# Kernel tuning notes

Hardware: AMD Instinct MI355X
Metric: run time of the kernel (lower is better)

The kernel has to match this reference:

```python
import jax, jax.numpy as jnp
import numpy as np

NEIGHBOUR = 3  # matches init_kwargs['neighbour']


def _conv2d(x, w, b=None, stride=1, pad=0):
    out = jax.lax.conv_general_dilated(
        x, w, (stride, stride), [(pad, pad), (pad, pad)],
        dimension_numbers=('NCHW', 'OIHW', 'NCHW'))
    if b is not None:
        out = out + b[None, :, None, None]
    return out


def _warp(x, offset, wg_w, wg_b, conv_w):
    """Deformable bilinear warp: offsets -> 4 corner gathers -> modulate -> regroup -> strided conv."""
    k = NEIGHBOUR
    N = k * k
    B, C, H, W = x.shape
    m = jax.nn.sigmoid(_conv2d(x, wg_w, wg_b, 1, 1))          # [B,N,H,W] modulation gate
    xp = jnp.pad(x, ((0, 0), (0, 0), (1, 1), (1, 1)))         # zero pad -> [B,C,H+2,W+2]
    Hp, Wp = H + 2, W + 2
    r = jnp.arange(-(k - 1) // 2, (k - 1) // 2 + 1, dtype=x.dtype)
    pnx, pny = jnp.meshgrid(r, r, indexing='ij')              # kernel-neighbour offsets p_n
    # absolute sampling positions in padded coords (p_0 starts at 1 due to padding)
    p0x = jnp.arange(1, H + 1, dtype=x.dtype)[None, :, None, None]
    p0y = jnp.arange(1, W + 1, dtype=x.dtype)[None, None, :, None]
    off = offset.transpose(0, 2, 3, 1)                        # [B,H,W,2N]; first N = x, last N = y
    px = p0x + pnx.ravel()[None, None, None, :] + off[..., :N]  # [B,H,W,N]
    py = p0y + pny.ravel()[None, None, None, :] + off[..., N:]
    fx = jnp.floor(jax.lax.stop_gradient(px))                 # p.detach().floor()
    fy = jnp.floor(jax.lax.stop_gradient(py))
    qx_lt = jnp.clip(fx, 0, Hp - 1)
    qy_lt = jnp.clip(fy, 0, Wp - 1)
    qx_rb = jnp.clip(fx + 1, 0, Hp - 1)
    qy_rb = jnp.clip(fy + 1, 0, Wp - 1)
    px = jnp.clip(px, 0, Hp - 1)
    py = jnp.clip(py, 0, Wp - 1)
    # bilinear weights (same algebra as the torch code)
    g_lt = (1 + (qx_lt - px)) * (1 + (qy_lt - py))
    g_rb = (1 - (qx_rb - px)) * (1 - (qy_rb - py))
    g_lb = (1 + (qx_lt - px)) * (1 - (qy_rb - py))
    g_rt = (1 - (qx_rb - px)) * (1 + (qy_lt - py))
    ix_lt = qx_lt.astype(jnp.int32); iy_lt = qy_lt.astype(jnp.int32)
    ix_rb = qx_rb.astype(jnp.int32); iy_rb = qy_rb.astype(jnp.int32)
    x_flat = xp.reshape(B, C, Hp * Wp)

    def gather(ix, iy):
        idx = (ix * Wp + iy).reshape(B, 1, H * W * N)
        return jnp.take_along_axis(x_flat, idx, axis=-1).reshape(B, C, H, W, N)

    xw = (g_lt[:, None] * gather(ix_lt, iy_lt)
          + g_rb[:, None] * gather(ix_rb, iy_rb)
          + g_lb[:, None] * gather(ix_lt, iy_rb)
          + g_rt[:, None] * gather(ix_rb, iy_lt))              # [B,C,H,W,N]
    xw = xw * m.transpose(0, 2, 3, 1)[:, None]                 # modulation, broadcast over C
    # regroup [B,C,H,W,k,k] -> [B,C,H*k,W*k] (matches _reshape_x_warped ordering)
    xw = xw.reshape(B, C, H, W, k, k).transpose(0, 1, 2, 4, 3, 5).reshape(B, C, H * k, W * k)
    return _conv2d(xw, conv_w, None, stride=k, pad=0)          # grouped-back strided conv


def setup_inputs() -> dict:
    B, C, MH, H, W = 4, 64, 18, 128, 128  # MH = 2*neighbour^2
    key = jax.random.key(0)
    ks = jax.random.split(key, 12)
    f32 = jnp.float32
    s = 0.05  # weight scale to keep gates unsaturated
    return {
        'x_t': jax.random.normal(ks[0], (B, C, H, W), f32),
        'pre_offset': jax.random.normal(ks[1], (B, MH, H, W), f32),
        'mean': jax.random.normal(ks[2], (B, MH, H, W), f32),
        'upd_w': s * jax.random.normal(ks[3], (MH, C + MH, 3, 3), f32),
        'upd_b': s * jax.random.normal(ks[4], (MH,), f32),
        'rst_w': s * jax.random.normal(ks[5], (MH, C + MH, 3, 3), f32),
        'rst_b': s * jax.random.normal(ks[6], (MH,), f32),
        'out_w': s * jax.random.normal(ks[7], (MH, C + MH, 3, 3), f32),
        'out_b': s * jax.random.normal(ks[8], (MH,), f32),
        'wg_w': s * jax.random.normal(ks[9], (9, C, 3, 3), f32),
        'wg_b': s * jax.random.normal(ks[10], (9,), f32),
        'warp_conv_w': s * jax.random.normal(ks[11], (C, C, 3, 3), f32),
    }


def reference(x_t, pre_offset, mean, upd_w, upd_b, rst_w, rst_b, out_w, out_b,
              wg_w, wg_b, warp_conv_w):
    stacked = jnp.concatenate([x_t, pre_offset], axis=1)
    update_gate = jax.nn.sigmoid(_conv2d(stacked, upd_w, upd_b, 1, 1))
    reset_gate = jax.nn.sigmoid(_conv2d(stacked, rst_w, rst_b, 1, 1))
    cand = jnp.tanh(_conv2d(jnp.concatenate([x_t, pre_offset * reset_gate], axis=1), out_w, out_b, 1, 1))
    offset = pre_offset * (1 - update_gate) + cand * update_gate
    mean_new = mean + 0.5 * (pre_offset - mean)
    offset = offset + mean_new
    x_out = _warp(x_t, offset, wg_w, wg_b, warp_conv_w)
    return (x_out, offset, mean_new)
```

## Files before the change

kernel.cpp:

```cpp
#include <hip/hip_runtime.h>
#include <hip/hip_bf16.h>
#include <math.h>

#define Bn  4
#define Cc  64
#define MHc 18
#define Hh  128
#define Wd  128
#define HW  (Hh*Wd)
#define Np  9
#define HP  130
#define WP  130
#define XPE (HP*WP*Cc)
#define PPE (HP*WP*32)
#define KX  576
#define KP  288
#define KT  (KX+KP)

typedef __attribute__((ext_vector_type(8))) short short8;
typedef __attribute__((ext_vector_type(4))) float float4v;

__device__ __forceinline__ float bf2f(__hip_bfloat16 x) { return __bfloat162float(x); }
__device__ __forceinline__ __hip_bfloat16 f2bf(float x) { return __float2bfloat16(x); }
__device__ __forceinline__ float sigm(float x) { return 1.f / (1.f + expf(-x)); }
__device__ __forceinline__ float s2f(short s) {
  return __uint_as_float(((unsigned)(unsigned short)s) << 16);
}
__device__ __forceinline__ short f2bs(float x) {
  __hip_bfloat16 h = __float2bfloat16(x);
  return *reinterpret_cast<short*>(&h);
}

#define NW1 (64*KT)
#define NW2 (32*KP)
#define NW3 (Cc*Cc*Np)

__global__ __launch_bounds__(256)
void k_prep(const float* __restrict__ x, const float* __restrict__ po,
            const float* __restrict__ upd_w, const float* __restrict__ rst_w,
            const float* __restrict__ out_w, const float* __restrict__ wg_w,
            const float* __restrict__ wcw,
            __hip_bfloat16* __restrict__ xp, __hip_bfloat16* __restrict__ pp,
            __hip_bfloat16* __restrict__ rp,
            __hip_bfloat16* __restrict__ wall, __hip_bfloat16* __restrict__ w2,
            __hip_bfloat16* __restrict__ wt) {
  __shared__ float tile[128][65];
  int blk = blockIdx.x;
  int t = threadIdx.x;
  if (blk < 512) {
    int b = blk >> 7, h = blk & 127;
    int c = t >> 2;
    int wbase = (t & 3) * 32;
    const float* src = &x[(b*Cc + c)*HW + h*Wd + wbase];
    #pragma unroll
    for (int j = 0; j < 8; ++j) {
      float4v v = *reinterpret_cast<const float4v*>(src + j*4);
      tile[wbase + j*4 + 0][c] = v.x;
      tile[wbase + j*4 + 1][c] = v.y;
      tile[wbase + j*4 + 2][c] = v.z;
      tile[wbase + j*4 + 3][c] = v.w;
    }
    __syncthreads();
    #pragma unroll
    for (int j = 0; j < 4; ++j) {
      int i = t + j * 256;
      int px = i >> 3, oct = i & 7;
      short8 ov;
      #pragma unroll
      for (int e = 0; e < 8; ++e) ov[e] = f2bs(tile[px][oct*8 + e]);
      *reinterpret_cast<short8*>(
          &xp[b*XPE + ((h+1)*WP + px + 1)*Cc + oct*8]) = ov;
    }
  } else if (blk < 1024) {
    int pb = blk - 512;
    int h = pb & 127;
    int b = pb >> 7;
    int w = t & 127;
    int half = t >> 7;
    float v[9];
    #pragma unroll
    for (int j = 0; j < 9; ++j)
      v[j] = po[(b*MHc + half*9 + j)*HW + h*Wd + w];
    #pragma unroll
    for (int j = 0; j < 9; ++j)
      pp[b*PPE + ((h+1)*WP + (w+1))*32 + half*9 + j] = f2bf(v[j]);
  } else if (blk < 1420) {
    int idx = (blk - 1024) * 256 + t;
    if (idx < NW1) {
      int k  = idx % KT;
      int gr = idx / KT;
      float v = 0.f;
      if (k < KX) {
        int n = k >> 6, ci = k & 63;
        if      (gr < 18) v = upd_w[(gr*(Cc+MHc) + ci)*9 + n];
        else if (gr < 36) v = rst_w[((gr-18)*(Cc+MHc) + ci)*9 + n];
        else if (gr < 54) v = out_w[((gr-36)*(Cc+MHc) + ci)*9 + n];
        else if (gr < 63) v = wg_w[((gr-54)*Cc + ci)*9 + n];
      } else {
        int kk = k - KX;
        int n = kk >> 5, jc = kk & 31;
        if (jc < 18) {
          if      (gr < 18) v = upd_w[(gr*(Cc+MHc) + Cc + jc)*9 + n];
          else if (gr < 36) v = rst_w[((gr-18)*(Cc+MHc) + Cc + jc)*9 + n];
        }
      }
      wall[idx] = f2bf(v);
    } else if (idx < NW1 + NW2) {
      int i2 = idx - NW1;
      int k  = i2 % KP;
      int oc = i2 / KP;
      int n = k >> 5, jc = k & 31;
      float v = (oc < 18 && jc < 18) ? out_w[(oc*(Cc+MHc) + Cc + jc)*9 + n] : 0.f;
      w2[i2] = f2bf(v);
    } else if (idx < NW1 + NW2 + NW3) {
      int i3 = idx - NW1 - NW2;
      int k  = i3 % 576;
      int co = i3 / 576;
      wt[i3] = f2bf(wcw[(co*Cc + (k & 63))*9 + (k >> 6)]);
    }
  } else {
    int bid = blk - 1420;
    int kind = bid >> 2;
    int b = bid & 3;
    short8 z = {0,0,0,0,0,0,0,0};
    if (kind == 0) {
      __hip_bfloat16* base = xp + b*XPE;
      for (int i = t; i < 4128; i += 256) {
        int off;
        if (i < 2080) {
          int row = (i < 1040) ? 0 : 129;
          int j = (i < 1040) ? i : i - 1040;
          off = row*130*64 + j*8;
        } else {
          int i2 = i - 2080;
          int strip = i2 >> 3;
          int r = 1 + (strip & 127);
          int side = strip >> 7;
          off = (r*130 + side*129)*64 + (i2 & 7)*8;
        }
        *reinterpret_cast<short8*>(base + off) = z;
      }
    } else {
      __hip_bfloat16* base = (kind == 1 ? pp : rp) + b*PPE;
      for (int i = t; i < 2064; i += 256) {
        int off;
        if (i < 1040) {
          int row = (i < 520) ? 0 : 129;
          int j = (i < 520) ? i : i - 520;
          off = row*130*32 + j*8;
        } else {
          int i2 = i - 1040;
          int strip = i2 >> 2;
          int r = 1 + (strip & 127);
          int side = strip >> 7;
          off = (r*130 + side*129)*32 + (i2 & 3)*8;
        }
        *reinterpret_cast<short8*>(base + off) = z;
      }
    }
  }
}

__global__ __launch_bounds__(256)
void k_gates(const __hip_bfloat16* __restrict__ xpad,
             const __hip_bfloat16* __restrict__ popad,
             const __hip_bfloat16* __restrict__ wall,
             const float* __restrict__ po,
             const float* __restrict__ upd_b,
             const float* __restrict__ rst_b,
             const float* __restrict__ out_b,
             const float* __restrict__ wg_b,
             float* __restrict__ u_out,
             float* __restrict__ cx_out,
             __hip_bfloat16* __restrict__ ropad,
             __hip_bfloat16* __restrict__ m_t) {
  __shared__ __align__(16) char winx[13056];
  __shared__ __align__(16) char winp[6528];
  __shared__ __align__(16) __hip_bfloat16 roL[32][32];
  int blk = blockIdx.x;
  int wtile = blk & 3;
  int h = (blk >> 2) & 127;
  int b = blk >> 9;
  int w0 = wtile * 32;
  int lane = threadIdx.x & 63;
  int wave = threadIdx.x >> 6;
  int t = threadIdx.x;

  ((unsigned int*)roL)[t] = 0u;
  ((unsigned int*)roL)[t + 256] = 0u;

  const __hip_bfloat16* xpb = xpad + b * XPE;
  const __hip_bfloat16* ppb = popad + b * PPE;

  for (int i = t; i < 816; i += 256) {
    int r = i / 272, cidx = i - r * 272;
    short8 v = *reinterpret_cast<const short8*>(
        xpb + ((h + r) * WP + w0) * Cc + cidx * 8);
    int o = i * 16;
    *reinterpret_cast<short8*>(winx + (o ^ (((o >> 7) & 7) << 4))) = v;
  }
  for (int i = t; i < 408; i += 256) {
    int r = i / 136, cidx = i - r * 136;
    short8 v = *reinterpret_cast<const short8*>(
        ppb + ((h + r) * WP + w0) * 32 + cidx * 8);
    int o = i * 16;
    *reinterpret_cast<short8*>(winp + (o ^ (((o >> 6) & 3) << 4))) = v;
  }
  __syncthreads();

  int mrow = lane & 15;
  int quad = lane >> 4;
  int cotile = wave * 16;
  float4v acc0 = {0.f, 0.f, 0.f, 0.f};
  float4v acc1 = {0.f, 0.f, 0.f, 0.f};
  #pragma unroll
  for (int ks = 0; ks < KT/32; ++ks) {
    short8 a = *reinterpret_cast<const short8*>(
        wall + (cotile + mrow) * KT + ks * 32 + quad * 8);
    short8 b0, b1;
    if (ks < 18) {
      int n = ks >> 1;
      int r0i = (n / 3) * 34 + mrow + (n % 3);
      int r1i = r0i + 16;
      int l0 = r0i * 128 + (ks & 1) * 64 + quad * 16;
      int l1 = r1i * 128 + (ks & 1) * 64 + quad * 16;
      b0 = *reinterpret_cast<const short8*>(winx + (l0 ^ ((r0i & 7) << 4)));
      b1 = *reinterpret_cast<const short8*>(winx + (l1 ^ ((r1i & 7) << 4)));
    } else {
      int n = ks - 18;
      int r0i = (n / 3) * 34 + mrow + (n % 3);
      int r1i = r0i + 16;
      int l0 = r0i * 64 + quad * 16;
      int l1 = r1i * 64 + quad * 16;
      b0 = *reinterpret_cast<const short8*>(winp + (l0 ^ ((r0i & 3) << 4)));
      b1 = *reinterpret_cast<const short8*>(winp + (l1 ^ ((r1i & 3) << 4)));
    }
    acc0 = __builtin_amdgcn_mfma_f32_16x16x32_bf16(a, b0, acc0, 0, 0, 0);
    acc1 = __builtin_amdgcn_mfma_f32_16x16x32_bf16(a, b1, acc1, 0, 0, 0);
  }

  int sp0 = h * Wd + w0 + mrow;
  int sp1 = sp0 + 16;
  float pv0[4], pv1[4];
  #pragma unroll
  for (int r = 0; r < 4; ++r) {
    int gr = cotile + quad * 4 + r;
    if (gr >= 18 && gr < 36) {
      pv0[r] = po[(b*MHc + (gr-18))*HW + sp0];
      pv1[r] = po[(b*MHc + (gr-18))*HW + sp1];
    }
  }
  #pragma unroll
  for (int r = 0; r < 4; ++r) {
    int gr = cotile + quad * 4 + r;
    float v0 = acc0[r], v1 = acc1[r];
    if (gr < 18) {
      u_out[(b*MHc + gr)*HW + sp0] = sigm(v0 + upd_b[gr]);
      u_out[(b*MHc + gr)*HW + sp1] = sigm(v1 + upd_b[gr]);
    } else if (gr < 36) {
      int oc = gr - 18;
      roL[mrow][oc]      = f2bf(sigm(v0 + rst_b[oc]) * pv0[r]);
      roL[16 + mrow][oc] = f2bf(sigm(v1 + rst_b[oc]) * pv1[r]);
    } else if (gr < 54) {
      int oc = gr - 36;
      cx_out[(b*MHc + oc)*HW + sp0] = v0 + out_b[oc];
      cx_out[(b*MHc + oc)*HW + sp1] = v1 + out_b[oc];
    } else if (gr < 63) {
      int nn = gr - 54;
      m_t[nn*(Bn*HW) + b*HW + sp0] = f2bf(sigm(v0 + wg_b[nn]));
      m_t[nn*(Bn*HW) + b*HW + sp1] = f2bf(sigm(v1 + wg_b[nn]));
    }
  }
  __syncthreads();
  unsigned int* dst = (unsigned int*)(ropad + b*PPE + ((h+1)*WP + (w0+1))*32);
  dst[t] = ((unsigned int*)roL)[t];
  dst[t + 256] = ((unsigned int*)roL)[t + 256];
}

__global__ __launch_bounds__(512, 6)
void k_fuse(const __hip_bfloat16* __restrict__ xpad,
            const __hip_bfloat16* __restrict__ ropad,
            const __hip_bfloat16* __restrict__ w2,
            const __hip_bfloat16* __restrict__ wt,
            const __hip_bfloat16* __restrict__ m_t,
            const float* __restrict__ po,
            const float* __restrict__ mean,
            float* __restrict__ out_off,
            float* __restrict__ out_mn,
            float* __restrict__ out_x) {
  __shared__ __align__(16) char lbuf[32*584*2];
  __shared__ float offL[32][18];
  __shared__ float mL[32][9];
  __shared__ __align__(16) float gw[288][4];
  __shared__ __align__(16) int   ga[288][2];
  auto xw = (__hip_bfloat16(*)[584])lbuf;

  int blk = blockIdx.x;
  int wtile = blk & 3;
  int h = (blk >> 2) & 127;
  int b = blk >> 9;
  int w0 = wtile * 32;
  int lane = threadIdx.x & 63;
  int wv = threadIdx.x >> 6;
  int t = threadIdx.x;
  int mrow = lane & 15;
  int quad = lane >> 4;

  float ov[4], uv[4], pv[4], mv[4];
  int gil[4];
  int am = wv & 1, pg = wv >> 1;
  if (wv < 4) {
    int sp = h * Wd + w0 + pg*16 + mrow;
    #pragma unroll
    for (int r = 0; r < 4; ++r) {
      int gr = am*16 + quad * 4 + r;
      gil[r] = (b*MHc + gr)*HW + sp;
      if (gr < 18) {
        ov[r] = out_off[gil[r]];
        uv[r] = out_mn[gil[r]];
        pv[r] = po[gil[r]];
        mv[r] = mean[gil[r]];
      }
    }
  }

  const __hip_bfloat16* rpb = ropad + b * PPE;
  if (t < 408) {
    int r = t / 136, cidx = t - r * 136;
    short8 v = *reinterpret_cast<const short8*>(
        rpb + ((h + r) * WP + w0) * 32 + cidx * 8);
    int o = t * 16;
    *reinterpret_cast<short8*>(lbuf + (o ^ (((o >> 6) & 3) << 4))) = v;
  }
  if (t < 288) {
    int n = t >> 5, px = t & 31;
    mL[px][n] = bf2f(m_t[n*(Bn*HW) + b*HW + h*Wd + w0 + px]);
  }
  __syncthreads();

  if (wv < 4) {
    float4v acc = {0.f, 0.f, 0.f, 0.f};
    #pragma unroll
    for (int ks = 0; ks < 9; ++ks) {
      short8 a = *reinterpret_cast<const short8*>(
          w2 + (am*16 + mrow) * KP + ks * 32 + quad * 8);
      int rowidx = (ks / 3) * 34 + pg*16 + mrow + (ks % 3);
      int lin = rowidx * 64 + quad * 16;
      short8 bfr = *reinterpret_cast<const short8*>(
          lbuf + (lin ^ ((rowidx & 3) << 4)));
      acc = __builtin_amdgcn_mfma_f32_16x16x32_bf16(a, bfr, acc, 0, 0, 0);
    }
    #pragma unroll
    for (int r = 0; r < 4; ++r) {
      int gr = am*16 + quad * 4 + r;
      if (gr < 18) {
        float cand = tanhf(ov[r] + acc[r]);
        float mn = 0.5f * (mv[r] + pv[r]);
        float off = pv[r] * (1.f - uv[r]) + cand * uv[r] + mn;
        out_off[gil[r]] = off;
        out_mn[gil[r]]  = mn;
        offL[pg*16 + mrow][gr] = off;
      }
    }
  }
  __syncthreads();

  if (t < 288) {
    int px = t / 9;
    int n = t - px * 9;
    int wp = w0 + px;
    float ox = offL[px][n];
    float oy = offL[px][9 + n];
    float mnv = mL[px][n];
    float px_ = (float)(h + 1) + (float)(n / 3 - 1) + ox;
    float py_ = (float)(wp + 1) + (float)(n % 3 - 1) + oy;
    float fx = floorf(px_), fy = floorf(py_);
    float xlt = fminf(fmaxf(fx,       0.f), 129.f);
    float ylt = fminf(fmaxf(fy,       0.f), 129.f);
    float xrb = fminf(fmaxf(fx + 1.f, 0.f), 129.f);
    float yrb = fminf(fmaxf(fy + 1.f, 0.f), 129.f);
    float pxc = fminf(fmaxf(px_, 0.f), 129.f);
    float pyc = fminf(fmaxf(py_, 0.f), 129.f);
    float glt = (1.f + xlt - pxc) * (1.f + ylt - pyc);
    float grb = (1.f - xrb + pxc) * (1.f - yrb + pyc);
    float glb = (1.f + xlt - pxc) * (1.f - yrb + pyc);
    float grt = (1.f - xrb + pxc) * (1.f + ylt - pyc);
    int ixl = (int)xlt, iyl = (int)ylt, ixr = (int)xrb, iyr = (int)yrb;
    bool yAdj = (iyr == iyl + 1);
    gw[t][0] = (glt + (yAdj ? 0.f : glb)) * mnv;
    gw[t][1] = (yAdj ? glb : 0.f) * mnv;
    gw[t][2] = (grt + (yAdj ? 0.f : grb)) * mnv;
    gw[t][3] = (yAdj ? grb : 0.f) * mnv;
    ga[t][0] = (ixl * WP + iyl) * Cc;
    ga[t][1] = (ixr * WP + iyl) * Cc;
  }
  __syncthreads();

  const __hip_bfloat16* xpb = xpad + b * XPE;
  for (int it = t; it < 2304; it += 512) {
    int q  = it >> 3;
    int c0 = (it & 7) * 8;
    float4v g = *reinterpret_cast<const float4v*>(gw[q]);
    int bL = ga[q][0] + c0, bR = ga[q][1] + c0;
    short8 l0 = *reinterpret_cast<const short8*>(xpb + bL);
    short8 l1 = *reinterpret_cast<const short8*>(xpb + bL + 64);
    short8 r0 = *reinterpret_cast<const short8*>(xpb + bR);
    short8 r1 = *reinterpret_cast<const short8*>(xpb + bR + 64);
    short8 ovv;
    #pragma unroll
    for (int j = 0; j < 8; ++j) {
      float vv = g.x * s2f(l0[j]);
      vv = fmaf(g.y, s2f(l1[j]), vv);
      vv = fmaf(g.z, s2f(r0[j]), vv);
      vv = fmaf(g.w, s2f(r1[j]), vv);
      ovv[j] = f2bs(vv);
    }
    int pl = q / 9;
    int n  = q - pl * 9;
    *reinterpret_cast<short8*>(&xw[pl][n * 64 + c0]) = ovv;
  }
  __syncthreads();

  int ct = wv & 3, pg5 = wv >> 2;
  float4v acc = {0.f, 0.f, 0.f, 0.f};
  for (int ks = 0; ks < 18; ++ks) {
    short8 a = *reinterpret_cast<const short8*>(
        wt + (ct*16 + mrow) * 576 + ks * 32 + quad * 8);
    short8 bfr = *reinterpret_cast<const short8*>(
        &xw[pg5*16 + mrow][ks * 32 + quad * 8]);
    acc = __builtin_amdgcn_mfma_f32_16x16x32_bf16(a, bfr, acc, 0, 0, 0);
  }
  #pragma unroll
  for (int r = 0; r < 4; ++r) {
    int co = ct*16 + quad * 4 + r;
    out_x[((b * Cc + co) * Hh + h) * Wd + w0 + pg5*16 + mrow] = acc[r];
  }
}

__global__ void f_convAB(const float* __restrict__ x, const float* __restrict__ po,
                         const float* __restrict__ wA, const float* __restrict__ bA,
                         const float* __restrict__ wB, const float* __restrict__ bB,
                         float* __restrict__ u_scr, float* __restrict__ ro_scr) {
  int idx = blockIdx.x * 256 + threadIdx.x;
  if (idx >= Bn * MHc * HW) return;
  int w = idx & 127, h = (idx >> 7) & 127, oc = (idx >> 14) % MHc, b = idx / (MHc*HW);
  float accA = bA[oc], accB = bB[oc];
  const float* xb = x + b*Cc*HW; const float* pb = po + b*MHc*HW;
  for (int ic = 0; ic < Cc + MHc; ++ic) {
    const float* src = (ic < Cc) ? (xb + ic*HW) : (pb + (ic-Cc)*HW);
    const float* wa = wA + (oc*(Cc+MHc)+ic)*9; const float* wb = wB + (oc*(Cc+MHc)+ic)*9;
    for (int kh = 0; kh < 3; ++kh) { int hh = h+kh-1; if ((unsigned)hh >= Hh) continue;
      for (int kw = 0; kw < 3; ++kw) { int ww = w+kw-1; if ((unsigned)ww >= Wd) continue;
        float v = src[hh*Wd+ww]; accA += v*wa[kh*3+kw]; accB += v*wb[kh*3+kw]; } }
  }
  u_scr[idx] = sigm(accA); ro_scr[idx] = sigm(accB) * pb[oc*HW + h*Wd + w];
}
__global__ void f_convC(const float* __restrict__ x, const float* __restrict__ po,
                        const float* __restrict__ mean, const float* __restrict__ wC,
                        const float* __restrict__ bC, const float* __restrict__ u_scr,
                        const float* __restrict__ ro_scr, float* __restrict__ out_off,
                        float* __restrict__ out_mean) {
  int idx = blockIdx.x * 256 + threadIdx.x;
  if (idx >= Bn * MHc * HW) return;
  int w = idx & 127, h = (idx >> 7) & 127, oc = (idx >> 14) % MHc, b = idx / (MHc*HW);
  float acc = bC[oc];
  const float* xb = x + b*Cc*HW; const float* rb = ro_scr + b*MHc*HW;
  for (int ic = 0; ic < Cc + MHc; ++ic) {
    const float* src = (ic < Cc) ? (xb + ic*HW) : (rb + (ic-Cc)*HW);
    const float* wv = wC + (oc*(Cc+MHc)+ic)*9;
    for (int kh = 0; kh < 3; ++kh) { int hh = h+kh-1; if ((unsigned)hh >= Hh) continue;
      for (int kw = 0; kw < 3; ++kw) { int ww = w+kw-1; if ((unsigned)ww >= Wd) continue;
        acc += src[hh*Wd+ww]*wv[kh*3+kw]; } }
  }
  float cand = tanhf(acc); float u = u_scr[idx]; float p = po[idx];
  float mn = 0.5f*(mean[idx]+p);
  out_off[idx] = p*(1.f-u)+cand*u+mn; out_mean[idx] = mn;
}
__global__ __launch_bounds__(256)
void f_warp(const float* __restrict__ x, const float* __restrict__ off_f,
            const float* __restrict__ wg, const float* __restrict__ bg,
            const float* __restrict__ wc, float* __restrict__ out) {
  __shared__ float mred[4][Np][64]; __shared__ float mval[4][Np];
  __shared__ float xwv[4][Np][64];
  int lane = threadIdx.x & 63, wave = threadIdx.x >> 6;
  int p = blockIdx.x * 4 + wave;
  int b = p >> 14, rem = p & 16383, h = rem >> 7, w = rem & 127;
  const float* xc = x + (b*Cc + lane)*HW;
  float part[Np];
  for (int n = 0; n < Np; ++n) part[n] = 0.f;
  for (int kh = 0; kh < 3; ++kh) { int hh = h+kh-1; if ((unsigned)hh >= Hh) continue;
    for (int kw = 0; kw < 3; ++kw) { int ww = w+kw-1; if ((unsigned)ww >= Wd) continue;
      float v = xc[hh*Wd+ww];
      for (int n = 0; n < Np; ++n) part[n] += v*wg[(n*Cc+lane)*9+kh*3+kw]; } }
  for (int n = 0; n < Np; ++n) mred[wave][n][lane] = part[n];
  __syncthreads();
  if (lane < Np) { float s = bg[lane];
    for (int c = 0; c < Cc; ++c) s += mred[wave][lane][c];
    mval[wave][lane] = sigm(s); }
  __syncthreads();
  const float* offb = off_f + b*MHc*HW; int sp = h*Wd + w;
  for (int n = 0; n < Np; ++n) {
    float px = (float)(h+1) + (float)(n/3-1) + offb[n*HW+sp];
    float py = (float)(w+1) + (float)(n%3-1) + offb[(9+n)*HW+sp];
    float fxq = floorf(px), fyq = floorf(py);
    float xlt = fminf(fmaxf(fxq,0.f),129.f), ylt = fminf(fmaxf(fyq,0.f),129.f);
    float xrb = fminf(fmaxf(fxq+1.f,0.f),129.f), yrb = fminf(fmaxf(fyq+1.f,0.f),129.f);
    float pxc = fminf(fmaxf(px,0.f),129.f), pyc = fminf(fmaxf(py,0.f),129.f);
    float glt = (1.f+xlt-pxc)*(1.f+ylt-pyc), grb = (1.f-xrb+pxc)*(1.f-yrb+pyc);
    float glb = (1.f+xlt-pxc)*(1.f-yrb+pyc), grt = (1.f-xrb+pxc)*(1.f+ylt-pyc);
    int ixl=(int)xlt, iyl=(int)ylt, ixr=(int)xrb, iyr=(int)yrb;
    float vlt=0.f,vrb=0.f,vlb=0.f,vrt=0.f;
    if (ixl>=1&&ixl<=Hh&&iyl>=1&&iyl<=Wd) vlt = xc[(ixl-1)*Wd+(iyl-1)];
    if (ixr>=1&&ixr<=Hh&&iyr>=1&&iyr<=Wd) vrb = xc[(ixr-1)*Wd+(iyr-1)];
    if (ixl>=1&&ixl<=Hh&&iyr>=1&&iyr<=Wd) vlb = xc[(ixl-1)*Wd+(iyr-1)];
    if (ixr>=1&&ixr<=Hh&&iyl>=1&&iyl<=Wd) vrt = xc[(ixr-1)*Wd+(iyl-1)];
    xwv[wave][n][lane] = (glt*vlt+grb*vrb+glb*vlb+grt*vrt)*mval[wave][n];
  }
  __syncthreads();
  float acc = 0.f;
  for (int c = 0; c < Cc; ++c)
    for (int n = 0; n < Np; ++n)
      acc += xwv[wave][n][c]*wc[(lane*Cc+c)*9+n];
  out[(b*Cc+lane)*HW + h*Wd + w] = acc;
}

extern "C" void kernel_launch(void* const* d_in, const int* in_sizes, int n_in,
                              void* d_out, int out_size, void* d_ws, size_t ws_size,
                              hipStream_t stream) {
  (void)in_sizes; (void)n_in; (void)out_size;
  const float* x_t   = (const float*)d_in[0];
  const float* po    = (const float*)d_in[1];
  const float* mean  = (const float*)d_in[2];
  const float* upd_w = (const float*)d_in[3];
  const float* upd_b = (const float*)d_in[4];
  const float* rst_w = (const float*)d_in[5];
  const float* rst_b = (const float*)d_in[6];
  const float* out_w = (const float*)d_in[7];
  const float* out_b = (const float*)d_in[8];
  const float* wg_w  = (const float*)d_in[9];
  const float* wg_b  = (const float*)d_in[10];
  const float* wcw   = (const float*)d_in[11];

  float* out_x   = (float*)d_out;
  float* out_off = out_x + 4194304;
  float* out_mn  = out_off + 1179648;

  char* ws = (char*)d_ws;
  __hip_bfloat16* xpad  = (__hip_bfloat16*)(ws + 0);
  __hip_bfloat16* popad = (__hip_bfloat16*)(ws + 8652800);
  __hip_bfloat16* ropad = (__hip_bfloat16*)(ws + 12979200);
  __hip_bfloat16* wall  = (__hip_bfloat16*)(ws + 17305600);
  __hip_bfloat16* w2    = (__hip_bfloat16*)(ws + 17416192);
  __hip_bfloat16* wt_bf = (__hip_bfloat16*)(ws + 17434624);
  __hip_bfloat16* m_t   = (__hip_bfloat16*)(ws + 17508352);
  const size_t WS_NEED = 18688000;

  if (ws_size >= WS_NEED) {
    hipLaunchKernelGGL(k_prep,  dim3(1432), dim3(256), 0, stream,
                       x_t, po, upd_w, rst_w, out_w, wg_w, wcw,
                       xpad, popad, ropad, wall, w2, wt_bf);
    hipLaunchKernelGGL(k_gates, dim3(2048), dim3(256), 0, stream,
                       xpad, popad, wall, po, upd_b, rst_b, out_b, wg_b,
                       out_mn, out_off, ropad, m_t);
    hipLaunchKernelGGL(k_fuse,  dim3(2048), dim3(512), 0, stream,
                       xpad, ropad, w2, wt_bf, m_t, po, mean,
                       out_off, out_mn, out_x);
  } else {
    float* u_scr  = out_x;
    float* cx_scr = out_x + 1179648;
    hipLaunchKernelGGL(f_convAB, dim3(4608), dim3(256), 0, stream,
                       x_t, po, upd_w, upd_b, rst_w, rst_b, u_scr, cx_scr);
    hipLaunchKernelGGL(f_convC,  dim3(4608), dim3(256), 0, stream,
                       x_t, po, mean, out_w, out_b, u_scr, cx_scr,
                       out_off, out_mn);
    hipLaunchKernelGGL(f_warp,   dim3(16384), dim3(256), 0, stream,
                       x_t, out_off, wg_w, wg_b, wcw, out_x);
  }
}
```

Before: 178.0 us.

## Process two rows per gates block and overlap warp gather with MFMA

k_gates now computes two output rows per block with four accumulator groups. This halves the grid, reuses the 3-row halo window across two rows (4 rows loaded instead of 6), and amortizes each weight fragment load over twice the MFMAs. k_fuse drops the LDS staging of the reset-offset window and reads B fragments directly from global memory. It also splits the bilinear gather so the first 4 neighbours are built before the final conv, while the remaining 5 are gathered in between the first 8 MFMA k-steps, overlapping memory latency with matrix work. The cost is higher register pressure from the extra accumulators and prefetched gathers, plus uncoalesced global reads in the small conv.

```diff
diff --git a/kernel.cpp b/kernel.cpp
--- a/kernel.cpp
+++ b/kernel.cpp
@@ -174,35 +174,37 @@
              float* __restrict__ cx_out,
              __hip_bfloat16* __restrict__ ropad,
              __hip_bfloat16* __restrict__ m_t) {
-  __shared__ __align__(16) char winx[13056];
-  __shared__ __align__(16) char winp[6528];
-  __shared__ __align__(16) __hip_bfloat16 roL[32][32];
+  __shared__ __align__(16) char winx[17408];
+  __shared__ __align__(16) char winp[8704];
+  __shared__ __align__(16) __hip_bfloat16 roL[64][32];
   int blk = blockIdx.x;
   int wtile = blk & 3;
-  int h = (blk >> 2) & 127;
-  int b = blk >> 9;
+  int hp = (blk >> 2) & 63;
+  int b = blk >> 8;
+  int h0 = hp * 2;
   int w0 = wtile * 32;
   int lane = threadIdx.x & 63;
   int wave = threadIdx.x >> 6;
   int t = threadIdx.x;
 
-  ((unsigned int*)roL)[t] = 0u;
-  ((unsigned int*)roL)[t + 256] = 0u;
+  #pragma unroll
+  for (int j = 0; j < 4; ++j)
+    ((unsigned int*)roL)[t + j*256] = 0u;
 
   const __hip_bfloat16* xpb = xpad + b * XPE;
   const __hip_bfloat16* ppb = popad + b * PPE;
 
-  for (int i = t; i < 816; i += 256) {
+  for (int i = t; i < 1088; i += 256) {
     int r = i / 272, cidx = i - r * 272;
     short8 v = *reinterpret_cast<const short8*>(
-        xpb + ((h + r) * WP + w0) * Cc + cidx * 8);
+        xpb + ((h0 + r) * WP + w0) * Cc + cidx * 8);
     int o = i * 16;
     *reinterpret_cast<short8*>(winx + (o ^ (((o >> 7) & 7) << 4))) = v;
   }
-  for (int i = t; i < 408; i += 256) {
+  for (int i = t; i < 544; i += 256) {
     int r = i / 136, cidx = i - r * 136;
     short8 v = *reinterpret_cast<const short8*>(
-        ppb + ((h + r) * WP + w0) * 32 + cidx * 8);
+        ppb + ((h0 + r) * WP + w0) * 32 + cidx * 8);
     int o = i * 16;
     *reinterpret_cast<short8*>(winp + (o ^ (((o >> 6) & 3) << 4))) = v;
   }
@@ -211,70 +213,81 @@
   int mrow = lane & 15;
   int quad = lane >> 4;
   int cotile = wave * 16;
-  float4v acc0 = {0.f, 0.f, 0.f, 0.f};
-  float4v acc1 = {0.f, 0.f, 0.f, 0.f};
+  float4v ac[4];
+  #pragma unroll
+  for (int g = 0; g < 4; ++g) ac[g] = (float4v){0.f,0.f,0.f,0.f};
+
   #pragma unroll
   for (int ks = 0; ks < KT/32; ++ks) {
     short8 a = *reinterpret_cast<const short8*>(
         wall + (cotile + mrow) * KT + ks * 32 + quad * 8);
-    short8 b0, b1;
     if (ks < 18) {
       int n = ks >> 1;
-      int r0i = (n / 3) * 34 + mrow + (n % 3);
-      int r1i = r0i + 16;
-      int l0 = r0i * 128 + (ks & 1) * 64 + quad * 16;
-      int l1 = r1i * 128 + (ks & 1) * 64 + quad * 16;
-      b0 = *reinterpret_cast<const short8*>(winx + (l0 ^ ((r0i & 7) << 4)));
-      b1 = *reinterpret_cast<const short8*>(winx + (l1 ^ ((r1i & 7) << 4)));
+      #pragma unroll
+      for (int g = 0; g < 4; ++g) {
+        int hh = g >> 1, pgi = g & 1;
+        int rowidx = (n / 3 + hh) * 34 + pgi*16 + mrow + (n % 3);
+        int lin = rowidx * 128 + (ks & 1) * 64 + quad * 16;
+        short8 bf = *reinterpret_cast<const short8*>(
+            winx + (lin ^ ((rowidx & 7) << 4)));
+        ac[g] = __builtin_amdgcn_mfma_f32_16x16x32_bf16(a, bf, ac[g], 0, 0, 0);
+      }
     } else {
       int n = ks - 18;
-      int r0i = (n / 3) * 34 + mrow + (n % 3);
-      int r1i = r0i + 16;
-      int l0 = r0i * 64 + quad * 16;
-      int l1 = r1i * 64 + quad * 16;
-      b0 = *reinterpret_cast<const short8*>(winp + (l0 ^ ((r0i & 3) << 4)));
-      b1 = *reinterpret_cast<const short8*>(winp + (l1 ^ ((r1i & 3) << 4)));
-    }
-    acc0 = __builtin_amdgcn_mfma_f32_16x16x32_bf16(a, b0, acc0, 0, 0, 0);
-    acc1 = __builtin_amdgcn_mfma_f32_16x16x32_bf16(a, b1, acc1, 0, 0, 0);
-  }
-
-  int sp0 = h * Wd + w0 + mrow;
-  int sp1 = sp0 + 16;
-  float pv0[4], pv1[4];
-  #pragma unroll
-  for (int r = 0; r < 4; ++r) {
-    int gr = cotile + quad * 4 + r;
-    if (gr >= 18 && gr < 36) {
-      pv0[r] = po[(b*MHc + (gr-18))*HW + sp0];
-      pv1[r] = po[(b*MHc + (gr-18))*HW + sp1];
-    }
-  }
-  #pragma unroll
-  for (int r = 0; r < 4; ++r) {
-    int gr = cotile + quad * 4 + r;
-    float v0 = acc0[r], v1 = acc1[r];
-    if (gr < 18) {
-      u_out[(b*MHc + gr)*HW + sp0] = sigm(v0 + upd_b[gr]);
-      u_out[(b*MHc + gr)*HW + sp1] = sigm(v1 + upd_b[gr]);
-    } else if (gr < 36) {
-      int oc = gr - 18;
-      roL[mrow][oc]      = f2bf(sigm(v0 + rst_b[oc]) * pv0[r]);
-      roL[16 + mrow][oc] = f2bf(sigm(v1 + rst_b[oc]) * pv1[r]);
-    } else if (gr < 54) {
-      int oc = gr - 36;
-      cx_out[(b*MHc + oc)*HW + sp0] = v0 + out_b[oc];
-      cx_out[(b*MHc + oc)*HW + sp1] = v1 + out_b[oc];
-    } else if (gr < 63) {
-      int nn = gr - 54;
-      m_t[nn*(Bn*HW) + b*HW + sp0] = f2bf(sigm(v0 + wg_b[nn]));
-      m_t[nn*(Bn*HW) + b*HW + sp1] = f2bf(sigm(v1 + wg_b[nn]));
-    }
-  }
-  __syncthreads();
-  unsigned int* dst = (unsigned int*)(ropad + b*PPE + ((h+1)*WP + (w0+1))*32);
-  dst[t] = ((unsigned int*)roL)[t];
-  dst[t + 256] = ((unsigned int*)roL)[t + 256];
+      #pragma unroll
+      for (int g = 0; g < 4; ++g) {
+        int hh = g >> 1, pgi = g & 1;
+        int rowidx = (n / 3 + hh) * 34 + pgi*16 + mrow + (n % 3);
+        int lin = rowidx * 64 + quad * 16;
+        short8 bf = *reinterpret_cast<const short8*>(
+            winp + (lin ^ ((rowidx & 3) << 4)));
+        ac[g] = __builtin_amdgcn_mfma_f32_16x16x32_bf16(a, bf, ac[g], 0, 0, 0);
+      }
+    }
+  }
+
+  float pvv[4][4];
+  #pragma unroll
+  for (int g = 0; g < 4; ++g) {
+    int hh = g >> 1, pgi = g & 1;
+    int sp = (h0 + hh) * Wd + w0 + pgi*16 + mrow;
+    #pragma unroll
+    for (int r = 0; r < 4; ++r) {
+      int gr = cotile + quad * 4 + r;
+      if (gr >= 18 && gr < 36)
+        pvv[g][r] = po[(b*MHc + (gr-18))*HW + sp];
+    }
+  }
+  #pragma unroll
+  for (int g = 0; g < 4; ++g) {
+    int hh = g >> 1, pgi = g & 1;
+    int sp = (h0 + hh) * Wd + w0 + pgi*16 + mrow;
+    #pragma unroll
+    for (int r = 0; r < 4; ++r) {
+      int gr = cotile + quad * 4 + r;
+      float v = ac[g][r];
+      if (gr < 18) {
+        u_out[(b*MHc + gr)*HW + sp] = sigm(v + upd_b[gr]);
+      } else if (gr < 36) {
+        int oc = gr - 18;
+        roL[hh*32 + pgi*16 + mrow][oc] = f2bf(sigm(v + rst_b[oc]) * pvv[g][r]);
+      } else if (gr < 54) {
+        int oc = gr - 36;
+        cx_out[(b*MHc + oc)*HW + sp] = v + out_b[oc];
+      } else if (gr < 63) {
+        int nn = gr - 54;
+        m_t[nn*(Bn*HW) + b*HW + sp] = f2bf(sigm(v + wg_b[nn]));
+      }
+    }
+  }
+  __syncthreads();
+  #pragma unroll
+  for (int hh = 0; hh < 2; ++hh) {
+    unsigned int* dst = (unsigned int*)(ropad + b*PPE + ((h0+1+hh)*WP + (w0+1))*32);
+    #pragma unroll
+    for (int k = 0; k < 2; ++k)
+      dst[t + k*256] = ((unsigned int*)roL)[hh*512 + t + k*256];
+  }
 }
 
 __global__ __launch_bounds__(512, 6)
@@ -288,12 +301,11 @@
             float* __restrict__ out_off,
             float* __restrict__ out_mn,
             float* __restrict__ out_x) {
-  __shared__ __align__(16) char lbuf[32*584*2];
+  __shared__ __align__(16) __hip_bfloat16 xw[32][584];
   __shared__ float offL[32][18];
   __shared__ float mL[32][9];
   __shared__ __align__(16) float gw[288][4];
   __shared__ __align__(16) int   ga[288][2];
-  auto xw = (__hip_bfloat16(*)[584])lbuf;
 
   int blk = blockIdx.x;
   int wtile = blk & 3;
@@ -323,31 +335,20 @@
       }
     }
   }
-
-  const __hip_bfloat16* rpb = ropad + b * PPE;
-  if (t < 408) {
-    int r = t / 136, cidx = t - r * 136;
-    short8 v = *reinterpret_cast<const short8*>(
-        rpb + ((h + r) * WP + w0) * 32 + cidx * 8);
-    int o = t * 16;
-    *reinterpret_cast<short8*>(lbuf + (o ^ (((o >> 6) & 3) << 4))) = v;
-  }
   if (t < 288) {
     int n = t >> 5, px = t & 31;
     mL[px][n] = bf2f(m_t[n*(Bn*HW) + b*HW + h*Wd + w0 + px]);
   }
-  __syncthreads();
 
   if (wv < 4) {
+    const __hip_bfloat16* rpb = ropad + b * PPE;
     float4v acc = {0.f, 0.f, 0.f, 0.f};
     #pragma unroll
     for (int ks = 0; ks < 9; ++ks) {
       short8 a = *reinterpret_cast<const short8*>(
           w2 + (am*16 + mrow) * KP + ks * 32 + quad * 8);
-      int rowidx = (ks / 3) * 34 + pg*16 + mrow + (ks % 3);
-      int lin = rowidx * 64 + quad * 16;
       short8 bfr = *reinterpret_cast<const short8*>(
-          lbuf + (lin ^ ((rowidx & 3) << 4)));
+          rpb + ((h + ks/3) * WP + w0 + pg*16 + mrow + ks%3) * 32 + quad * 8);
       acc = __builtin_amdgcn_mfma_f32_16x16x32_bf16(a, bfr, acc, 0, 0, 0);
     }
     #pragma unroll
@@ -397,9 +398,12 @@
   __syncthreads();
 
   const __hip_bfloat16* xpb = xpad + b * XPE;
-  for (int it = t; it < 2304; it += 512) {
-    int q  = it >> 3;
-    int c0 = (it & 7) * 8;
+  #pragma unroll
+  for (int rep = 0; rep < 2; ++rep) {
+    int it = t + rep * 512;
+    int qi = it >> 3, c0 = (it & 7) * 8;
+    int px = qi >> 2, n = qi & 3;
+    int q = px * 9 + n;
     float4v g = *reinterpret_cast<const float4v*>(gw[q]);
     int bL = ga[q][0] + c0, bR = ga[q][1] + c0;
     short8 l0 = *reinterpret_cast<const short8*>(xpb + bL);
@@ -415,19 +419,115 @@
       vv = fmaf(g.w, s2f(r1[j]), vv);
       ovv[j] = f2bs(vv);
     }
-    int pl = q / 9;
-    int n  = q - pl * 9;
-    *reinterpret_cast<short8*>(&xw[pl][n * 64 + c0]) = ovv;
+    *reinterpret_cast<short8*>(&xw[px][n * 64 + c0]) = ovv;
   }
   __syncthreads();
 
   int ct = wv & 3, pg5 = wv >> 2;
+  const __hip_bfloat16* wtw = wt + (ct*16 + mrow) * 576;
+  int xrow = pg5*16 + mrow;
   float4v acc = {0.f, 0.f, 0.f, 0.f};
-  for (int ks = 0; ks < 18; ++ks) {
-    short8 a = *reinterpret_cast<const short8*>(
-        wt + (ct*16 + mrow) * 576 + ks * 32 + quad * 8);
-    short8 bfr = *reinterpret_cast<const short8*>(
-        &xw[pg5*16 + mrow][ks * 32 + quad * 8]);
+
+  int qi0 = t >> 3, c00 = (t & 7) * 8;
+  int px0 = qi0 / 5, n0 = 4 + (qi0 - px0 * 5);
+  int q0 = px0 * 9 + n0;
+  float4v g0 = *reinterpret_cast<const float4v*>(gw[q0]);
+  int bL0 = ga[q0][0] + c00, bR0 = ga[q0][1] + c00;
+  short8 A00 = *reinterpret_cast<const short8*>(xpb + bL0);
+  short8 A10 = *reinterpret_cast<const short8*>(xpb + bL0 + 64);
+  short8 A20 = *reinterpret_cast<const short8*>(xpb + bR0);
+  short8 A30 = *reinterpret_cast<const short8*>(xpb + bR0 + 64);
+
+  #pragma unroll
+  for (int ks = 0; ks < 4; ++ks) {
+    short8 a = *reinterpret_cast<const short8*>(wtw + ks * 32 + quad * 8);
+    short8 bfr = *reinterpret_cast<const short8*>(&xw[xrow][ks * 32 + quad * 8]);
+    acc = __builtin_amdgcn_mfma_f32_16x16x32_bf16(a, bfr, acc, 0, 0, 0);
+  }
+
+  {
+    short8 ovv;
+    #pragma unroll
+    for (int j = 0; j < 8; ++j) {
+      float vv = g0.x * s2f(A00[j]);
+      vv = fmaf(g0.y, s2f(A10[j]), vv);
+      vv = fmaf(g0.z, s2f(A20[j]), vv);
+      vv = fmaf(g0.w, s2f(A30[j]), vv);
+      ovv[j] = f2bs(vv);
+    }
+    *reinterpret_cast<short8*>(&xw[px0][n0 * 64 + c00]) = ovv;
+  }
+  int it1 = t + 512;
+  int qi1 = it1 >> 3, c01 = (it1 & 7) * 8;
+  int px1 = qi1 / 5, n1 = 4 + (qi1 - px1 * 5);
+  int q1 = px1 * 9 + n1;
+  float4v g1 = *reinterpret_cast<const float4v*>(gw[q1]);
+  int bL1 = ga[q1][0] + c01, bR1 = ga[q1][1] + c01;
+  short8 A01 = *reinterpret_cast<const short8*>(xpb + bL1);
+  short8 A11 = *reinterpret_cast<const short8*>(xpb + bL1 + 64);
+  short8 A21 = *reinterpret_cast<const short8*>(xpb + bR1);
+  short8 A31 = *reinterpret_cast<const short8*>(xpb + bR1 + 64);
+
+  #pragma unroll
+  for (int ks = 4; ks < 6; ++ks) {
+    short8 a = *reinterpret_cast<const short8*>(wtw + ks * 32 + quad * 8);
+    short8 bfr = *reinterpret_cast<const short8*>(&xw[xrow][ks * 32 + quad * 8]);
+    acc = __builtin_amdgcn_mfma_f32_16x16x32_bf16(a, bfr, acc, 0, 0, 0);
+  }
+
+  {
+    short8 ovv;
+    #pragma unroll
+    for (int j = 0; j < 8; ++j) {
+      float vv = g1.x * s2f(A01[j]);
+      vv = fmaf(g1.y, s2f(A11[j]), vv);
+      vv = fmaf(g1.z, s2f(A21[j]), vv);
+      vv = fmaf(g1.w, s2f(A31[j]), vv);
+      ovv[j] = f2bs(vv);
+    }
+    *reinterpret_cast<short8*>(&xw[px1][n1 * 64 + c01]) = ovv;
+  }
+  bool ok2 = (t < 256);
+  int it2 = t + 1024;
+  int qi2 = it2 >> 3, c02 = (it2 & 7) * 8;
+  int px2 = qi2 / 5, n2 = 4 + (qi2 - px2 * 5);
+  int q2 = px2 * 9 + n2;
+  float4v g2 = {0.f,0.f,0.f,0.f};
+  short8 A02, A12, A22, A32;
+  if (ok2) {
+    g2 = *reinterpret_cast<const float4v*>(gw[q2]);
+    int bL2 = ga[q2][0] + c02, bR2 = ga[q2][1] + c02;
+    A02 = *reinterpret_cast<const short8*>(xpb + bL2);
+    A12 = *reinterpret_cast<const short8*>(xpb + bL2 + 64);
+    A22 = *reinterpret_cast<const short8*>(xpb + bR2);
+    A32 = *reinterpret_cast<const short8*>(xpb + bR2 + 64);
+  }
+
+  #pragma unroll
+  for (int ks = 6; ks < 8; ++ks) {
+    short8 a = *reinterpret_cast<const short8*>(wtw + ks * 32 + quad * 8);
+    short8 bfr = *reinterpret_cast<const short8*>(&xw[xrow][ks * 32 + quad * 8]);
+    acc = __builtin_amdgcn_mfma_f32_16x16x32_bf16(a, bfr, acc, 0, 0, 0);
+  }
+
+  if (ok2) {
+    short8 ovv;
+    #pragma unroll
+    for (int j = 0; j < 8; ++j) {
+      float vv = g2.x * s2f(A02[j]);
+      vv = fmaf(g2.y, s2f(A12[j]), vv);
+      vv = fmaf(g2.z, s2f(A22[j]), vv);
+      vv = fmaf(g2.w, s2f(A32[j]), vv);
+      ovv[j] = f2bs(vv);
+    }
+    *reinterpret_cast<short8*>(&xw[px2][n2 * 64 + c02]) = ovv;
+  }
+  __syncthreads();
+
+  #pragma unroll
+  for (int ks = 8; ks < 18; ++ks) {
+    short8 a = *reinterpret_cast<const short8*>(wtw + ks * 32 + quad * 8);
+    short8 bfr = *reinterpret_cast<const short8*>(&xw[xrow][ks * 32 + quad * 8]);
     acc = __builtin_amdgcn_mfma_f32_16x16x32_bf16(a, bfr, acc, 0, 0, 0);
   }
   #pragma unroll
@@ -559,7 +659,7 @@
     hipLaunchKernelGGL(k_prep,  dim3(1432), dim3(256), 0, stream,
                        x_t, po, upd_w, rst_w, out_w, wg_w, wcw,
                        xpad, popad, ropad, wall, w2, wt_bf);
-    hipLaunchKernelGGL(k_gates, dim3(2048), dim3(256), 0, stream,
+    hipLaunchKernelGGL(k_gates, dim3(1024), dim3(256), 0, stream,
                        xpad, popad, wall, po, upd_b, rst_b, out_b, wg_b,
                        out_mn, out_off, ropad, m_t);
     hipLaunchKernelGGL(k_fuse,  dim3(2048), dim3(512), 0, stream,
```

Result: slower. 184.0 us (+3.4%).
